# Kernel optimization log

Measured on AMD Instinct MI355X. Metric: run time of the kernel, lower is better.

Reference implementation:

```python
import jax, jax.numpy as jnp
import numpy as np

B, F = 64, 2048

def setup_inputs() -> dict:
    key = jax.random.key(0)
    k1, k2, k3, k4, k5 = jax.random.split(key, 5)
    scale = 1.0 / np.sqrt(F)
    return {
        "x": jax.random.normal(k1, (B, F), dtype=jnp.float32),
        "feature_mask": jax.random.randint(k2, (B, F), 0, 2, dtype=jnp.int32),
        "Wq": jax.random.normal(k3, (F, F), dtype=jnp.float32) * scale,
        "Wk": jax.random.normal(k4, (F, F), dtype=jnp.float32) * scale,
        "Wv": jax.random.normal(k5, (F, F), dtype=jnp.float32) * scale,
    }

def reference(x, feature_mask, Wq, Wk, Wv):
    # nn.Linear(bias=False): y = x @ W.T
    q = x @ Wq.T  # (B, F)
    k = x @ Wk.T
    v = x @ Wv.T
    # outer-product scores: (B, F, F) = q[:, :, None] * k[:, None, :]
    scores = q[:, :, None] * k[:, None, :]
    # mask broadcast over query dim (unsqueeze(1) in torch)
    scores = jnp.where(feature_mask[:, None, :] == 0, -1e9, scores)
    attn = jax.nn.softmax(scores, axis=-1)  # (B, F, F)
    attended = jnp.einsum("bfg,bg->bf", attn, v)  # (B, F)
    return attended
```

## Files before the change

kernel.cpp:

```cpp
#include <hip/hip_runtime.h>
#include <hip/hip_bf16.h>

#define B 64
#define F 2048
#define BN 64
#define BK 32
#define KSPLIT 8
#define KCHUNK (F / KSPLIT)
#define NITER (KCHUNK / BK)
#define LDSW 40
#define GS 4
#define NSEG 4

typedef __attribute__((ext_vector_type(8))) short bf16x8;
typedef __attribute__((ext_vector_type(4))) float f32x4;

#define PART_FLOATS (KSPLIT * 3 * B * F)
#define KVC_FLOATS (B * 2 * F)

#if __has_builtin(__builtin_amdgcn_exp2f)
#define EXP2(x) __builtin_amdgcn_exp2f(x)
#else
#define EXP2(x) exp2f(x)
#endif

__device__ __forceinline__ void split2(float f0, float f1, int& hi, int& lo) {
  union { float f; unsigned u; } a, b;
  a.f = f0; b.f = f1;
  union { unsigned u; float f; } ha, hb;
  ha.u = a.u & 0xFFFF0000u;
  hb.u = b.u & 0xFFFF0000u;
  union { float f; unsigned u; } la, lb;
  la.f = f0 - ha.f;
  lb.f = f1 - hb.f;
  hi = (int)__builtin_amdgcn_perm(b.u, a.u, 0x07060302u);
  lo = (int)__builtin_amdgcn_perm(lb.u, la.u, 0x07060302u);
}

__global__ __launch_bounds__(256) void qkv_gemm_kernel(
    const float* __restrict__ x, const float* __restrict__ Wq,
    const float* __restrict__ Wk, const float* __restrict__ Wv,
    float* __restrict__ part) {
  __shared__ __align__(16) short xs_hi[2][B][LDSW];
  __shared__ __align__(16) short xs_lo[2][B][LDSW];
  __shared__ __align__(16) short ws_hi[2][BN][LDSW];
  __shared__ __align__(16) short ws_lo[2][BN][LDSW];

  const int tid  = threadIdx.x;
  const int f0   = blockIdx.x * BN;
  const int kb   = blockIdx.y;
  const int mat  = blockIdx.z;
  const float* W = (mat == 0) ? Wq : (mat == 1) ? Wk : Wv;

  const int lrow = tid >> 2;
  const int lc0  = (tid & 3) << 3;

  const int wave = tid >> 6;
  const int lane = tid & 63;
  const int l15  = lane & 15;
  const int quad = lane >> 4;

  const float* xg = x + lrow * F + kb * KCHUNK + lc0;
  const float* wg = W + (f0 + lrow) * F + kb * KCHUNK + lc0;

  f32x4 acc[4];
#pragma unroll
  for (int i = 0; i < 4; ++i) acc[i] = (f32x4){0.f, 0.f, 0.f, 0.f};

  float4 px[2][2], pw[2][2];
  px[0][0] = *(const float4*)(xg);
  px[0][1] = *(const float4*)(xg + 4);
  pw[0][0] = *(const float4*)(wg);
  pw[0][1] = *(const float4*)(wg + 4);

#pragma unroll
  for (int it = 0; it < NITER; ++it) {
    const int cur = it & 1, nxt = cur ^ 1;
    if (it + 1 < NITER) {
      const float* xp = xg + (it + 1) * BK;
      const float* wp = wg + (it + 1) * BK;
      px[nxt][0] = *(const float4*)(xp);
      px[nxt][1] = *(const float4*)(xp + 4);
      pw[nxt][0] = *(const float4*)(wp);
      pw[nxt][1] = *(const float4*)(wp + 4);
    }
    int4 xh, xl, wh, wl;
    split2(px[cur][0].x, px[cur][0].y, xh.x, xl.x);
    split2(px[cur][0].z, px[cur][0].w, xh.y, xl.y);
    split2(px[cur][1].x, px[cur][1].y, xh.z, xl.z);
    split2(px[cur][1].z, px[cur][1].w, xh.w, xl.w);
    split2(pw[cur][0].x, pw[cur][0].y, wh.x, wl.x);
    split2(pw[cur][0].z, pw[cur][0].w, wh.y, wl.y);
    split2(pw[cur][1].x, pw[cur][1].y, wh.z, wl.z);
    split2(pw[cur][1].z, pw[cur][1].w, wh.w, wl.w);
    *(int4*)&xs_hi[cur][lrow][lc0] = xh;
    *(int4*)&xs_lo[cur][lrow][lc0] = xl;
    *(int4*)&ws_hi[cur][lrow][lc0] = wh;
    *(int4*)&ws_lo[cur][lrow][lc0] = wl;
    __syncthreads();

    bf16x8 a_hi = *(const bf16x8*)&xs_hi[cur][(wave << 4) + l15][quad << 3];
    bf16x8 a_lo = *(const bf16x8*)&xs_lo[cur][(wave << 4) + l15][quad << 3];
#pragma unroll
    for (int nt = 0; nt < 4; ++nt) {
      bf16x8 b_hi = *(const bf16x8*)&ws_hi[cur][(nt << 4) + l15][quad << 3];
      bf16x8 b_lo = *(const bf16x8*)&ws_lo[cur][(nt << 4) + l15][quad << 3];
      acc[nt] = __builtin_amdgcn_mfma_f32_16x16x32_bf16(a_hi, b_hi, acc[nt], 0, 0, 0);
      acc[nt] = __builtin_amdgcn_mfma_f32_16x16x32_bf16(a_hi, b_lo, acc[nt], 0, 0, 0);
      acc[nt] = __builtin_amdgcn_mfma_f32_16x16x32_bf16(a_lo, b_hi, acc[nt], 0, 0, 0);
    }
  }

  float* outp = part + (size_t)(kb * 3 + mat) * B * F;
#pragma unroll
  for (int nt = 0; nt < 4; ++nt) {
    int f = f0 + (nt << 4) + l15;
#pragma unroll
    for (int r = 0; r < 4; ++r) {
      int brow = (wave << 4) + (quad << 2) + r;
      outp[brow * F + f] = acc[nt][r];
    }
  }
}

__global__ __launch_bounds__(256) void prep_kernel(
    const float* __restrict__ part, const int* __restrict__ mask,
    float* __restrict__ kvc, float* __restrict__ vsum4,
    float* __restrict__ kmax4, float* __restrict__ kmin4,
    int* __restrict__ cnt4) {
  __shared__ int cnt;
  __shared__ float svs[4], smx[4], smn[4];

  const int b    = blockIdx.x;
  const int seg  = blockIdx.y;
  const int tid  = threadIdx.x;
  const int wave = tid >> 6;
  const int lane = tid & 63;

  if (tid == 0) cnt = 0;
  __syncthreads();

  float vs = 0.f, kmx = -3.4e38f, kmn = 3.4e38f;
  float* kvb = kvc + (size_t)b * 2 * F + seg * 1024;

#pragma unroll
  for (int c = wave; c < 8; c += 4) {
    int g = seg * 512 + (c << 6) + lane;
    float kg = 0.f, vg = 0.f;
#pragma unroll
    for (int p = 0; p < KSPLIT; ++p) {
      kg += part[((p * 3 + 1) * B + b) * F + g];
      vg += part[((p * 3 + 2) * B + b) * F + g];
    }
    vs += vg;
    bool act = (mask[b * F + g] != 0);
    unsigned long long bal = __ballot(act);
    int nw = __popcll(bal);
    int base = 0;
    if (lane == 0) base = atomicAdd(&cnt, nw);
    base = __shfl(base, 0);
    if (act) {
      int pos = base + __popcll(bal & ((1ull << lane) - 1ull));
      kvb[2 * pos]     = kg;
      kvb[2 * pos + 1] = vg;
      kmx = fmaxf(kmx, kg);
      kmn = fminf(kmn, kg);
    }
  }
#pragma unroll
  for (int o = 32; o > 0; o >>= 1) {
    vs += __shfl_xor(vs, o);
    kmx = fmaxf(kmx, __shfl_xor(kmx, o));
    kmn = fminf(kmn, __shfl_xor(kmn, o));
  }
  if (lane == 0) { svs[wave] = vs; smx[wave] = kmx; smn[wave] = kmn; }
  __syncthreads();
  if (tid == 0) {
    vsum4[b * NSEG + seg] = svs[0] + svs[1] + svs[2] + svs[3];
    kmax4[b * NSEG + seg] = fmaxf(fmaxf(smx[0], smx[1]), fmaxf(smx[2], smx[3]));
    kmin4[b * NSEG + seg] = fminf(fminf(smn[0], smn[1]), fminf(smn[2], smn[3]));
    cnt4[b * NSEG + seg]  = cnt;
  }
}

__global__ __launch_bounds__(1024, 8) void attn_kernel(
    const float* __restrict__ part, const float* __restrict__ kvc,
    const float* __restrict__ vsum4, const float* __restrict__ kmax4,
    const float* __restrict__ kming4, const int* __restrict__ cnt4,
    float* __restrict__ out) {
  __shared__ __align__(16) float kvs[4096];
  __shared__ float rn[GS][256];
  __shared__ float rd[GS][256];

  const int b     = blockIdx.x;
  const int tid   = threadIdx.x;
  const int fl    = tid & 255;
  const int slice = tid >> 8;
  const int fi    = blockIdx.y * 256 + fl;

  ((float4*)kvs)[tid] = ((const float4*)(kvc + (size_t)b * 2 * F))[tid];

  float s = 0.f;
#pragma unroll
  for (int p = 0; p < KSPLIT; ++p) s += part[((p * 3 + 0) * B + b) * F + fi];

  int cnts[NSEG];
  float km = -3.4e38f, kn = 3.4e38f;
  int ntot = 0;
  float vstot = 0.f;
#pragma unroll
  for (int g4 = 0; g4 < NSEG; ++g4) {
    cnts[g4] = cnt4[b * NSEG + g4];
    ntot += cnts[g4];
    km = fmaxf(km, kmax4[b * NSEG + g4]);
    kn = fminf(kn, kming4[b * NSEG + g4]);
    vstot += vsum4[b * NSEG + g4];
  }

  const float L2E = 1.44269504088896f;
  const float se  = s * L2E;
  const float nm2 = -se * ((s >= 0.f) ? km : kn);

  __syncthreads();

  float n0 = 0.f, n1 = 0.f, n2 = 0.f, n3 = 0.f;
  float d0 = 0.f, d1 = 0.f, d2 = 0.f, d3 = 0.f;
#pragma unroll
  for (int seg = 0; seg < NSEG; ++seg) {
    const int cnt   = cnts[seg];
    const int quads = cnt >> 1;
    const int q0 = (slice * quads) / GS;
    const int q1 = ((slice + 1) * quads) / GS;
    const float* base = kvs + (seg << 10);
    int q = q0;
    for (; q + 4 <= q1; q += 4) {
      float4 p0 = *(const float4*)(base + 4 * q);
      float4 p1 = *(const float4*)(base + 4 * q + 4);
      float4 p2 = *(const float4*)(base + 4 * q + 8);
      float4 p3 = *(const float4*)(base + 4 * q + 12);
      float e0 = EXP2(fmaf(se, p0.x, nm2));
      float e1 = EXP2(fmaf(se, p0.z, nm2));
      float e2 = EXP2(fmaf(se, p1.x, nm2));
      float e3 = EXP2(fmaf(se, p1.z, nm2));
      float e4 = EXP2(fmaf(se, p2.x, nm2));
      float e5 = EXP2(fmaf(se, p2.z, nm2));
      float e6 = EXP2(fmaf(se, p3.x, nm2));
      float e7 = EXP2(fmaf(se, p3.z, nm2));
      n0 = fmaf(e0, p0.y, n0); d0 += e0;
      n1 = fmaf(e1, p0.w, n1); d1 += e1;
      n2 = fmaf(e2, p1.y, n2); d2 += e2;
      n3 = fmaf(e3, p1.w, n3); d3 += e3;
      n0 = fmaf(e4, p2.y, n0); d0 += e4;
      n1 = fmaf(e5, p2.w, n1); d1 += e5;
      n2 = fmaf(e6, p3.y, n2); d2 += e6;
      n3 = fmaf(e7, p3.w, n3); d3 += e7;
    }
    for (; q < q1; ++q) {
      float4 p0 = *(const float4*)(base + 4 * q);
      float e0 = EXP2(fmaf(se, p0.x, nm2));
      float e1 = EXP2(fmaf(se, p0.z, nm2));
      n0 = fmaf(e0, p0.y, n0); d0 += e0;
      n1 = fmaf(e1, p0.w, n1); d1 += e1;
    }
    if ((slice == GS - 1) && (cnt & 1)) {
      float2 p = *(const float2*)(base + 2 * (cnt - 1));
      float e = EXP2(fmaf(se, p.x, nm2));
      n2 = fmaf(e, p.y, n2); d2 += e;
    }
  }
  rn[slice][fl] = (n0 + n1) + (n2 + n3);
  rd[slice][fl] = (d0 + d1) + (d2 + d3);
  __syncthreads();
  if (slice == 0) {
    float N = (rn[0][fl] + rn[1][fl]) + (rn[2][fl] + rn[3][fl]);
    float D = (rd[0][fl] + rd[1][fl]) + (rd[2][fl] + rd[3][fl]);
    out[b * F + fi] = (ntot > 0) ? (N / D) : (vstot * (1.0f / (float)F));
  }
}

extern "C" void kernel_launch(void* const* d_in, const int* in_sizes, int n_in,
                              void* d_out, int out_size, void* d_ws, size_t ws_size,
                              hipStream_t stream) {
  const float* x  = (const float*)d_in[0];
  const int* mask = (const int*)d_in[1];
  const float* Wq = (const float*)d_in[2];
  const float* Wk = (const float*)d_in[3];
  const float* Wv = (const float*)d_in[4];
  float* out = (float*)d_out;

  float* part  = (float*)d_ws;
  float* kvc   = part + PART_FLOATS;
  float* vsum4 = kvc + KVC_FLOATS;
  float* kmx4  = vsum4 + B * NSEG;
  float* kmn4  = kmx4 + B * NSEG;
  int*   cnt4  = (int*)(kmn4 + B * NSEG);

  dim3 gg(F / BN, KSPLIT, 3);
  qkv_gemm_kernel<<<gg, 256, 0, stream>>>(x, Wq, Wk, Wv, part);
  dim3 gp(B, NSEG);
  prep_kernel<<<gp, 256, 0, stream>>>(part, mask, kvc, vsum4, kmx4, kmn4, cnt4);
  dim3 ga(B, F / 256);
  attn_kernel<<<ga, 1024, 0, stream>>>(part, kvc, vsum4, kmx4, kmn4, cnt4, out);
}
```

Before: 124.0 us.

## Read compacted kv from global instead of LDS and vectorize prep with two segments

The prep kernel now processes 1024 features per block with float4 loads of partial sums and mask, using four ballots per wave and float2 stores of compacted (k,v) pairs. The attention kernel no longer stages the compacted kv buffer into shared memory and drops the barrier; instead each wave reads wave-uniform float4 values from global memory, with the slice index made scalar via readfirstlane. This removes LDS fill and sync cost and halves the number of per-batch segments, but relies on cache hits for the repeated global reads.

```diff
diff --git a/kernel.cpp b/kernel.cpp
--- a/kernel.cpp
+++ b/kernel.cpp
@@ -10,7 +10,8 @@
 #define NITER (KCHUNK / BK)
 #define LDSW 40
 #define GS 4
-#define NSEG 4
+#define NSEG 2
+#define SEGG 1024
 
 typedef __attribute__((ext_vector_type(8))) short bf16x8;
 typedef __attribute__((ext_vector_type(4))) float f32x4;
@@ -125,9 +126,9 @@
 
 __global__ __launch_bounds__(256) void prep_kernel(
     const float* __restrict__ part, const int* __restrict__ mask,
-    float* __restrict__ kvc, float* __restrict__ vsum4,
-    float* __restrict__ kmax4, float* __restrict__ kmin4,
-    int* __restrict__ cnt4) {
+    float* __restrict__ kvc, float* __restrict__ vsum2,
+    float* __restrict__ kmax2, float* __restrict__ kmin2,
+    int* __restrict__ cnt2) {
   __shared__ int cnt;
   __shared__ float svs[4], smx[4], smn[4];
 
@@ -140,33 +141,48 @@
   if (tid == 0) cnt = 0;
   __syncthreads();
 
-  float vs = 0.f, kmx = -3.4e38f, kmn = 3.4e38f;
-  float* kvb = kvc + (size_t)b * 2 * F + seg * 1024;
-
-#pragma unroll
-  for (int c = wave; c < 8; c += 4) {
-    int g = seg * 512 + (c << 6) + lane;
-    float kg = 0.f, vg = 0.f;
-#pragma unroll
-    for (int p = 0; p < KSPLIT; ++p) {
-      kg += part[((p * 3 + 1) * B + b) * F + g];
-      vg += part[((p * 3 + 2) * B + b) * F + g];
-    }
-    vs += vg;
-    bool act = (mask[b * F + g] != 0);
-    unsigned long long bal = __ballot(act);
-    int nw = __popcll(bal);
-    int base = 0;
-    if (lane == 0) base = atomicAdd(&cnt, nw);
-    base = __shfl(base, 0);
-    if (act) {
-      int pos = base + __popcll(bal & ((1ull << lane) - 1ull));
-      kvb[2 * pos]     = kg;
-      kvb[2 * pos + 1] = vg;
-      kmx = fmaxf(kmx, kg);
-      kmn = fminf(kmn, kg);
-    }
-  }
+  const int g0 = seg * SEGG + (tid << 2);
+  float4 kq = {0.f, 0.f, 0.f, 0.f}, vq = {0.f, 0.f, 0.f, 0.f};
+#pragma unroll
+  for (int p = 0; p < KSPLIT; ++p) {
+    const float4 kp = *(const float4*)&part[((p * 3 + 1) * B + b) * F + g0];
+    const float4 vp = *(const float4*)&part[((p * 3 + 2) * B + b) * F + g0];
+    kq.x += kp.x; kq.y += kp.y; kq.z += kp.z; kq.w += kp.w;
+    vq.x += vp.x; vq.y += vp.y; vq.z += vp.z; vq.w += vp.w;
+  }
+  float vs = (vq.x + vq.y) + (vq.z + vq.w);
+
+  const int4 m4 = *(const int4*)&mask[b * F + g0];
+  const float kk[4] = {kq.x, kq.y, kq.z, kq.w};
+  const float vv[4] = {vq.x, vq.y, vq.z, vq.w};
+  const bool  act[4] = {m4.x != 0, m4.y != 0, m4.z != 0, m4.w != 0};
+
+  unsigned long long bal[4];
+  int tot = 0;
+#pragma unroll
+  for (int j = 0; j < 4; ++j) {
+    bal[j] = __ballot(act[j]);
+    tot += __popcll(bal[j]);
+  }
+  int base = 0;
+  if (lane == 0) base = atomicAdd(&cnt, tot);
+  base = __shfl(base, 0);
+
+  float* kvb = kvc + (size_t)b * 2 * F + seg * 2 * SEGG;
+  const unsigned long long ltm = (1ull << lane) - 1ull;
+  float kmx = -3.4e38f, kmn = 3.4e38f;
+  int off = base;
+#pragma unroll
+  for (int j = 0; j < 4; ++j) {
+    if (act[j]) {
+      int pos = off + __popcll(bal[j] & ltm);
+      *(float2*)&kvb[2 * pos] = (float2){kk[j], vv[j]};
+      kmx = fmaxf(kmx, kk[j]);
+      kmn = fminf(kmn, kk[j]);
+    }
+    off += __popcll(bal[j]);
+  }
+
 #pragma unroll
   for (int o = 32; o > 0; o >>= 1) {
     vs += __shfl_xor(vs, o);
@@ -176,29 +192,26 @@
   if (lane == 0) { svs[wave] = vs; smx[wave] = kmx; smn[wave] = kmn; }
   __syncthreads();
   if (tid == 0) {
-    vsum4[b * NSEG + seg] = svs[0] + svs[1] + svs[2] + svs[3];
-    kmax4[b * NSEG + seg] = fmaxf(fmaxf(smx[0], smx[1]), fmaxf(smx[2], smx[3]));
-    kmin4[b * NSEG + seg] = fminf(fminf(smn[0], smn[1]), fminf(smn[2], smn[3]));
-    cnt4[b * NSEG + seg]  = cnt;
+    vsum2[b * NSEG + seg] = svs[0] + svs[1] + svs[2] + svs[3];
+    kmax2[b * NSEG + seg] = fmaxf(fmaxf(smx[0], smx[1]), fmaxf(smx[2], smx[3]));
+    kmin2[b * NSEG + seg] = fminf(fminf(smn[0], smn[1]), fminf(smn[2], smn[3]));
+    cnt2[b * NSEG + seg]  = cnt;
   }
 }
 
 __global__ __launch_bounds__(1024, 8) void attn_kernel(
     const float* __restrict__ part, const float* __restrict__ kvc,
-    const float* __restrict__ vsum4, const float* __restrict__ kmax4,
-    const float* __restrict__ kming4, const int* __restrict__ cnt4,
+    const float* __restrict__ vsum2, const float* __restrict__ kmax2,
+    const float* __restrict__ kmin2, const int* __restrict__ cnt2,
     float* __restrict__ out) {
-  __shared__ __align__(16) float kvs[4096];
   __shared__ float rn[GS][256];
   __shared__ float rd[GS][256];
 
   const int b     = blockIdx.x;
   const int tid   = threadIdx.x;
   const int fl    = tid & 255;
-  const int slice = tid >> 8;
+  const int slice = __builtin_amdgcn_readfirstlane(tid >> 8);
   const int fi    = blockIdx.y * 256 + fl;
-
-  ((float4*)kvs)[tid] = ((const float4*)(kvc + (size_t)b * 2 * F))[tid];
 
   float s = 0.f;
 #pragma unroll
@@ -209,35 +222,34 @@
   int ntot = 0;
   float vstot = 0.f;
 #pragma unroll
-  for (int g4 = 0; g4 < NSEG; ++g4) {
-    cnts[g4] = cnt4[b * NSEG + g4];
-    ntot += cnts[g4];
-    km = fmaxf(km, kmax4[b * NSEG + g4]);
-    kn = fminf(kn, kming4[b * NSEG + g4]);
-    vstot += vsum4[b * NSEG + g4];
+  for (int g2 = 0; g2 < NSEG; ++g2) {
+    cnts[g2] = cnt2[b * NSEG + g2];
+    ntot += cnts[g2];
+    km = fmaxf(km, kmax2[b * NSEG + g2]);
+    kn = fminf(kn, kmin2[b * NSEG + g2]);
+    vstot += vsum2[b * NSEG + g2];
   }
 
   const float L2E = 1.44269504088896f;
   const float se  = s * L2E;
   const float nm2 = -se * ((s >= 0.f) ? km : kn);
 
-  __syncthreads();
-
   float n0 = 0.f, n1 = 0.f, n2 = 0.f, n3 = 0.f;
   float d0 = 0.f, d1 = 0.f, d2 = 0.f, d3 = 0.f;
+  const float* kvbase = kvc + (size_t)b * 2 * F;
 #pragma unroll
   for (int seg = 0; seg < NSEG; ++seg) {
     const int cnt   = cnts[seg];
     const int quads = cnt >> 1;
     const int q0 = (slice * quads) / GS;
     const int q1 = ((slice + 1) * quads) / GS;
-    const float* base = kvs + (seg << 10);
+    const float4* bp = (const float4*)(kvbase + seg * 2 * SEGG);
     int q = q0;
     for (; q + 4 <= q1; q += 4) {
-      float4 p0 = *(const float4*)(base + 4 * q);
-      float4 p1 = *(const float4*)(base + 4 * q + 4);
-      float4 p2 = *(const float4*)(base + 4 * q + 8);
-      float4 p3 = *(const float4*)(base + 4 * q + 12);
+      float4 p0 = bp[q];
+      float4 p1 = bp[q + 1];
+      float4 p2 = bp[q + 2];
+      float4 p3 = bp[q + 3];
       float e0 = EXP2(fmaf(se, p0.x, nm2));
       float e1 = EXP2(fmaf(se, p0.z, nm2));
       float e2 = EXP2(fmaf(se, p1.x, nm2));
@@ -256,14 +268,14 @@
       n3 = fmaf(e7, p3.w, n3); d3 += e7;
     }
     for (; q < q1; ++q) {
-      float4 p0 = *(const float4*)(base + 4 * q);
+      float4 p0 = bp[q];
       float e0 = EXP2(fmaf(se, p0.x, nm2));
       float e1 = EXP2(fmaf(se, p0.z, nm2));
       n0 = fmaf(e0, p0.y, n0); d0 += e0;
       n1 = fmaf(e1, p0.w, n1); d1 += e1;
     }
     if ((slice == GS - 1) && (cnt & 1)) {
-      float2 p = *(const float2*)(base + 2 * (cnt - 1));
+      float2 p = *(const float2*)(kvbase + seg * 2 * SEGG + 2 * (cnt - 1));
       float e = EXP2(fmaf(se, p.x, nm2));
       n2 = fmaf(e, p.y, n2); d2 += e;
     }
@@ -290,15 +302,15 @@
 
   float* part  = (float*)d_ws;
   float* kvc   = part + PART_FLOATS;
-  float* vsum4 = kvc + KVC_FLOATS;
-  float* kmx4  = vsum4 + B * NSEG;
-  float* kmn4  = kmx4 + B * NSEG;
-  int*   cnt4  = (int*)(kmn4 + B * NSEG);
+  float* vsum2 = kvc + KVC_FLOATS;
+  float* kmx2  = vsum2 + B * NSEG;
+  float* kmn2  = kmx2 + B * NSEG;
+  int*   cnt2  = (int*)(kmn2 + B * NSEG);
 
   dim3 gg(F / BN, KSPLIT, 3);
   qkv_gemm_kernel<<<gg, 256, 0, stream>>>(x, Wq, Wk, Wv, part);
   dim3 gp(B, NSEG);
-  prep_kernel<<<gp, 256, 0, stream>>>(part, mask, kvc, vsum4, kmx4, kmn4, cnt4);
+  prep_kernel<<<gp, 256, 0, stream>>>(part, mask, kvc, vsum2, kmx2, kmn2, cnt2);
   dim3 ga(B, F / 256);
-  attn_kernel<<<ga, 1024, 0, stream>>>(part, kvc, vsum4, kmx4, kmn4, cnt4, out);
-}
+  attn_kernel<<<ga, 1024, 0, stream>>>(part, kvc, vsum2, kmx2, kmn2, cnt2, out);
+}
```

New measurement: 122.0 us. Within noise of the previous version (-1.6%).

## Fuse prep into GEMM via last-arriver atomic tickets; precompute q; read kv from global

Applied to the files above, without the earlier changes.

Folds the prep kernel into the QKV GEMM kernel. Each block takes an atomic ticket per 512-feature segment, and the last 64 arriving blocks wait on a ready counter, then reduce the split-K partials and compact the masked k/v pairs. The fused prep also sums q once into a qs buffer, so attn_kernel no longer reduces eight partials per thread. attn_kernel drops its LDS staging of kv and reads it straight from global/cache. This saves one launch and some redundant reads, but adds a spin-wait that depends on all producer blocks being resident or finished, plus a memset launch.

```diff
diff --git a/kernel.cpp b/kernel.cpp
--- a/kernel.cpp
+++ b/kernel.cpp
@@ -11,12 +11,14 @@
 #define LDSW 40
 #define GS 4
 #define NSEG 4
+#define RPROD 192
 
 typedef __attribute__((ext_vector_type(8))) short bf16x8;
 typedef __attribute__((ext_vector_type(4))) float f32x4;
 
 #define PART_FLOATS (KSPLIT * 3 * B * F)
 #define KVC_FLOATS (B * 2 * F)
+#define QS_FLOATS (B * F)
 
 #if __has_builtin(__builtin_amdgcn_exp2f)
 #define EXP2(x) __builtin_amdgcn_exp2f(x)
@@ -37,14 +39,21 @@
   lo = (int)__builtin_amdgcn_perm(lb.u, la.u, 0x07060302u);
 }
 
-__global__ __launch_bounds__(256) void qkv_gemm_kernel(
+__global__ __launch_bounds__(256) void qkv_gemm_prep_kernel(
     const float* __restrict__ x, const float* __restrict__ Wq,
     const float* __restrict__ Wk, const float* __restrict__ Wv,
-    float* __restrict__ part) {
+    const int* __restrict__ mask,
+    float* __restrict__ part, float* __restrict__ kvc,
+    float* __restrict__ qs, float* __restrict__ vsum4,
+    float* __restrict__ kmax4, float* __restrict__ kmin4,
+    int* __restrict__ cnt4, int* __restrict__ ready) {
   __shared__ __align__(16) short xs_hi[2][B][LDSW];
   __shared__ __align__(16) short xs_lo[2][B][LDSW];
   __shared__ __align__(16) short ws_hi[2][BN][LDSW];
   __shared__ __align__(16) short ws_lo[2][BN][LDSW];
+  __shared__ int ticket;
+  __shared__ int pcnt;
+  __shared__ float svs[4], smx[4], smn[4];
 
   const int tid  = threadIdx.x;
   const int f0   = blockIdx.x * BN;
@@ -121,52 +130,66 @@
       outp[brow * F + f] = acc[nt][r];
     }
   }
-}
-
-__global__ __launch_bounds__(256) void prep_kernel(
-    const float* __restrict__ part, const int* __restrict__ mask,
-    float* __restrict__ kvc, float* __restrict__ vsum4,
-    float* __restrict__ kmax4, float* __restrict__ kmin4,
-    int* __restrict__ cnt4) {
-  __shared__ int cnt;
-  __shared__ float svs[4], smx[4], smn[4];
-
-  const int b    = blockIdx.x;
-  const int seg  = blockIdx.y;
-  const int tid  = threadIdx.x;
-  const int wave = tid >> 6;
-  const int lane = tid & 63;
-
-  if (tid == 0) cnt = 0;
-  __syncthreads();
-
-  float vs = 0.f, kmx = -3.4e38f, kmn = 3.4e38f;
-  float* kvb = kvc + (size_t)b * 2 * F + seg * 1024;
-
-#pragma unroll
-  for (int c = wave; c < 8; c += 4) {
-    int g = seg * 512 + (c << 6) + lane;
-    float kg = 0.f, vg = 0.f;
-#pragma unroll
-    for (int p = 0; p < KSPLIT; ++p) {
-      kg += part[((p * 3 + 1) * B + b) * F + g];
-      vg += part[((p * 3 + 2) * B + b) * F + g];
-    }
-    vs += vg;
-    bool act = (mask[b * F + g] != 0);
-    unsigned long long bal = __ballot(act);
-    int nw = __popcll(bal);
-    int base = 0;
-    if (lane == 0) base = atomicAdd(&cnt, nw);
-    base = __shfl(base, 0);
-    if (act) {
-      int pos = base + __popcll(bal & ((1ull << lane) - 1ull));
-      kvb[2 * pos]     = kg;
-      kvb[2 * pos + 1] = vg;
-      kmx = fmaxf(kmx, kg);
-      kmn = fminf(kmn, kg);
-    }
-  }
+
+  const int seg = blockIdx.x >> 3;
+  __syncthreads();
+  if (tid == 0) {
+    __threadfence();
+    ticket = atomicAdd(&ready[seg], 1);
+  }
+  __syncthreads();
+  const int old = ticket;
+  if (old < RPROD - B) return;
+  const int b = old - (RPROD - B);
+
+  if (tid == 0) {
+    while (__hip_atomic_load(ready + seg, __ATOMIC_ACQUIRE,
+                             __HIP_MEMORY_SCOPE_AGENT) < RPROD) {
+      __builtin_amdgcn_s_sleep(2);
+    }
+    pcnt = 0;
+  }
+  __syncthreads();
+  __threadfence();
+
+  const int g0 = (seg << 9) + (tid << 1);
+  float2 kq = {0.f, 0.f}, vq = {0.f, 0.f}, qq = {0.f, 0.f};
+#pragma unroll
+  for (int p = 0; p < KSPLIT; ++p) {
+    const float* pb = part + (size_t)p * 3 * B * F + (size_t)b * F + g0;
+    const float2 q2 = *(const float2*)(pb);
+    const float2 k2 = *(const float2*)(pb + (size_t)B * F);
+    const float2 v2 = *(const float2*)(pb + (size_t)2 * B * F);
+    qq.x += q2.x; qq.y += q2.y;
+    kq.x += k2.x; kq.y += k2.y;
+    vq.x += v2.x; vq.y += v2.y;
+  }
+  *(float2*)&qs[b * F + g0] = qq;
+  float vs = vq.x + vq.y;
+
+  const int2 m2 = *(const int2*)&mask[b * F + g0];
+  const bool a0 = (m2.x != 0), a1 = (m2.y != 0);
+  const unsigned long long bal0 = __ballot(a0);
+  const unsigned long long bal1 = __ballot(a1);
+  const int tot = __popcll(bal0) + __popcll(bal1);
+  int basep = 0;
+  if (lane == 0) basep = atomicAdd(&pcnt, tot);
+  basep = __shfl(basep, 0);
+
+  float* kvb = kvc + (size_t)b * 2 * F + (seg << 10);
+  const unsigned long long ltm = (1ull << lane) - 1ull;
+  float kmx = -3.4e38f, kmn = 3.4e38f;
+  if (a0) {
+    int pos = basep + __popcll(bal0 & ltm);
+    *(float2*)&kvb[2 * pos] = (float2){kq.x, vq.x};
+    kmx = fmaxf(kmx, kq.x); kmn = fminf(kmn, kq.x);
+  }
+  if (a1) {
+    int pos = basep + __popcll(bal0) + __popcll(bal1 & ltm);
+    *(float2*)&kvb[2 * pos] = (float2){kq.y, vq.y};
+    kmx = fmaxf(kmx, kq.y); kmn = fminf(kmn, kq.y);
+  }
+
 #pragma unroll
   for (int o = 32; o > 0; o >>= 1) {
     vs += __shfl_xor(vs, o);
@@ -176,33 +199,28 @@
   if (lane == 0) { svs[wave] = vs; smx[wave] = kmx; smn[wave] = kmn; }
   __syncthreads();
   if (tid == 0) {
-    vsum4[b * NSEG + seg] = svs[0] + svs[1] + svs[2] + svs[3];
-    kmax4[b * NSEG + seg] = fmaxf(fmaxf(smx[0], smx[1]), fmaxf(smx[2], smx[3]));
-    kmin4[b * NSEG + seg] = fminf(fminf(smn[0], smn[1]), fminf(smn[2], smn[3]));
-    cnt4[b * NSEG + seg]  = cnt;
+    vsum4[(b << 2) + seg] = svs[0] + svs[1] + svs[2] + svs[3];
+    kmax4[(b << 2) + seg] = fmaxf(fmaxf(smx[0], smx[1]), fmaxf(smx[2], smx[3]));
+    kmin4[(b << 2) + seg] = fminf(fminf(smn[0], smn[1]), fminf(smn[2], smn[3]));
+    cnt4[(b << 2) + seg]  = pcnt;
   }
 }
 
 __global__ __launch_bounds__(1024, 8) void attn_kernel(
-    const float* __restrict__ part, const float* __restrict__ kvc,
+    const float* __restrict__ qs, const float* __restrict__ kvc,
     const float* __restrict__ vsum4, const float* __restrict__ kmax4,
-    const float* __restrict__ kming4, const int* __restrict__ cnt4,
+    const float* __restrict__ kmin4, const int* __restrict__ cnt4,
     float* __restrict__ out) {
-  __shared__ __align__(16) float kvs[4096];
   __shared__ float rn[GS][256];
   __shared__ float rd[GS][256];
 
   const int b     = blockIdx.x;
   const int tid   = threadIdx.x;
   const int fl    = tid & 255;
-  const int slice = tid >> 8;
+  const int slice = __builtin_amdgcn_readfirstlane(tid >> 8);
   const int fi    = blockIdx.y * 256 + fl;
 
-  ((float4*)kvs)[tid] = ((const float4*)(kvc + (size_t)b * 2 * F))[tid];
-
-  float s = 0.f;
-#pragma unroll
-  for (int p = 0; p < KSPLIT; ++p) s += part[((p * 3 + 0) * B + b) * F + fi];
+  const float s = qs[b * F + fi];
 
   int cnts[NSEG];
   float km = -3.4e38f, kn = 3.4e38f;
@@ -210,34 +228,33 @@
   float vstot = 0.f;
 #pragma unroll
   for (int g4 = 0; g4 < NSEG; ++g4) {
-    cnts[g4] = cnt4[b * NSEG + g4];
+    cnts[g4] = cnt4[(b << 2) + g4];
     ntot += cnts[g4];
-    km = fmaxf(km, kmax4[b * NSEG + g4]);
-    kn = fminf(kn, kming4[b * NSEG + g4]);
-    vstot += vsum4[b * NSEG + g4];
+    km = fmaxf(km, kmax4[(b << 2) + g4]);
+    kn = fminf(kn, kmin4[(b << 2) + g4]);
+    vstot += vsum4[(b << 2) + g4];
   }
 
   const float L2E = 1.44269504088896f;
   const float se  = s * L2E;
   const float nm2 = -se * ((s >= 0.f) ? km : kn);
 
-  __syncthreads();
-
   float n0 = 0.f, n1 = 0.f, n2 = 0.f, n3 = 0.f;
   float d0 = 0.f, d1 = 0.f, d2 = 0.f, d3 = 0.f;
+  const float* kvbase = kvc + (size_t)b * 2 * F;
 #pragma unroll
   for (int seg = 0; seg < NSEG; ++seg) {
     const int cnt   = cnts[seg];
     const int quads = cnt >> 1;
     const int q0 = (slice * quads) / GS;
     const int q1 = ((slice + 1) * quads) / GS;
-    const float* base = kvs + (seg << 10);
+    const float4* bp = (const float4*)(kvbase + (seg << 10));
     int q = q0;
     for (; q + 4 <= q1; q += 4) {
-      float4 p0 = *(const float4*)(base + 4 * q);
-      float4 p1 = *(const float4*)(base + 4 * q + 4);
-      float4 p2 = *(const float4*)(base + 4 * q + 8);
-      float4 p3 = *(const float4*)(base + 4 * q + 12);
+      float4 p0 = bp[q];
+      float4 p1 = bp[q + 1];
+      float4 p2 = bp[q + 2];
+      float4 p3 = bp[q + 3];
       float e0 = EXP2(fmaf(se, p0.x, nm2));
       float e1 = EXP2(fmaf(se, p0.z, nm2));
       float e2 = EXP2(fmaf(se, p1.x, nm2));
@@ -256,14 +273,14 @@
       n3 = fmaf(e7, p3.w, n3); d3 += e7;
     }
     for (; q < q1; ++q) {
-      float4 p0 = *(const float4*)(base + 4 * q);
+      float4 p0 = bp[q];
       float e0 = EXP2(fmaf(se, p0.x, nm2));
       float e1 = EXP2(fmaf(se, p0.z, nm2));
       n0 = fmaf(e0, p0.y, n0); d0 += e0;
       n1 = fmaf(e1, p0.w, n1); d1 += e1;
     }
     if ((slice == GS - 1) && (cnt & 1)) {
-      float2 p = *(const float2*)(base + 2 * (cnt - 1));
+      float2 p = *(const float2*)(kvbase + (seg << 10) + 2 * (cnt - 1));
       float e = EXP2(fmaf(se, p.x, nm2));
       n2 = fmaf(e, p.y, n2); d2 += e;
     }
@@ -290,15 +307,18 @@
 
   float* part  = (float*)d_ws;
   float* kvc   = part + PART_FLOATS;
-  float* vsum4 = kvc + KVC_FLOATS;
+  float* qs    = kvc + KVC_FLOATS;
+  float* vsum4 = qs + QS_FLOATS;
   float* kmx4  = vsum4 + B * NSEG;
   float* kmn4  = kmx4 + B * NSEG;
   int*   cnt4  = (int*)(kmn4 + B * NSEG);
+  int*   ready = cnt4 + B * NSEG;
+
+  hipMemsetAsync(ready, 0, NSEG * sizeof(int), stream);
 
   dim3 gg(F / BN, KSPLIT, 3);
-  qkv_gemm_kernel<<<gg, 256, 0, stream>>>(x, Wq, Wk, Wv, part);
-  dim3 gp(B, NSEG);
-  prep_kernel<<<gp, 256, 0, stream>>>(part, mask, kvc, vsum4, kmx4, kmn4, cnt4);
+  qkv_gemm_prep_kernel<<<gg, 256, 0, stream>>>(x, Wq, Wk, Wv, mask, part, kvc,
+                                               qs, vsum4, kmx4, kmn4, cnt4, ready);
   dim3 ga(B, F / 256);
-  attn_kernel<<<ga, 1024, 0, stream>>>(part, kvc, vsum4, kmx4, kmn4, cnt4, out);
+  attn_kernel<<<ga, 1024, 0, stream>>>(qs, kvc, vsum4, kmx4, kmn4, cnt4, out);
 }
```

Result: slower. 192.0 us (+54.8%).
